# Kernel optimization log

Hardware: AMD Instinct MI355X
Metric: run time of the kernel (lower is better)

The kernel has to match this reference:

```python
import math
import jax, jax.numpy as jnp
from jax import lax
import numpy as np

B, DIM, H, W = 8, 256, 64, 64
D_STATE, D_CONV, EXPAND = 16, 4, 2
D_INNER = EXPAND * DIM
DT_RANK = math.ceil(DIM / 16)
POS_LEN = 16
EPS = 1e-5
GN_GROUPS = 32


def setup_inputs() -> dict:
    key = jax.random.key(0)
    ks = iter(jax.random.split(key, 24))
    rn = lambda shape, s=0.02: jax.random.normal(next(ks), shape, jnp.float32) * s
    inp = {}
    inp["x"] = jax.random.normal(next(ks), (B, DIM, H, W), jnp.float32)
    inp["pos_emb"] = rn((1, DIM, POS_LEN), 1.0)
    inp["ln_g"] = jnp.ones((DIM,), jnp.float32)
    inp["ln_b"] = jnp.zeros((DIM,), jnp.float32)
    inp["m_in_w"] = rn((2, 2 * D_INNER, DIM))
    inp["m_conv_w"] = rn((2, D_INNER, D_CONV), 0.1)
    inp["m_conv_b"] = jnp.zeros((2, D_INNER), jnp.float32)
    inp["m_xproj_w"] = rn((2, DT_RANK + 2 * D_STATE, D_INNER))
    inp["m_dt_w"] = rn((2, D_INNER, DT_RANK), 0.1)
    inp["m_dt_b"] = rn((2, D_INNER), 0.1)
    inp["m_A_log"] = jnp.tile(jnp.log(jnp.arange(1, D_STATE + 1, dtype=jnp.float32))[None, None, :], (2, D_INNER, 1))
    inp["m_D"] = jnp.ones((2, D_INNER), jnp.float32)
    inp["m_out_w"] = rn((2, DIM, D_INNER))
    inp["proj_w"] = rn((DIM, 2 * DIM))
    inp["proj_b"] = jnp.zeros((DIM,), jnp.float32)
    inp["up_dw_w"] = rn((DIM, 1, 3, 3), 0.1)
    inp["up_bn1_g"] = jnp.ones((DIM,), jnp.float32)
    inp["up_bn1_b"] = jnp.zeros((DIM,), jnp.float32)
    inp["up_pw_w"] = rn((DIM, DIM), 0.05)
    inp["up_bn2_g"] = jnp.ones((DIM,), jnp.float32)
    inp["up_bn2_b"] = jnp.zeros((DIM,), jnp.float32)
    inp["down_pw_w"] = rn((DIM, DIM), 0.05)
    inp["down_bn_g"] = jnp.ones((DIM,), jnp.float32)
    inp["down_bn_b"] = jnp.zeros((DIM,), jnp.float32)
    inp["gn_g"] = jnp.ones((DIM,), jnp.float32)
    inp["gn_b"] = jnp.zeros((DIM,), jnp.float32)
    return inp


def reference(x, pos_emb, ln_g, ln_b, m_in_w, m_conv_w, m_conv_b, m_xproj_w, m_dt_w, m_dt_b,
              m_A_log, m_D, m_out_w, proj_w, proj_b, up_dw_w, up_bn1_g, up_bn1_b, up_pw_w,
              up_bn2_g, up_bn2_b, down_pw_w, down_bn_g, down_bn_b, gn_g, gn_b):
    Bx, C, Hh, Ww = x.shape

    def ln(t):  # LayerNorm over last dim (shared self.norm)
        m = jnp.mean(t, -1, keepdims=True)
        v = jnp.mean((t - m) ** 2, -1, keepdims=True)
        return (t - m) * lax.rsqrt(v + EPS) * ln_g + ln_b

    def bn(t, g, b):  # BatchNorm2d in eval mode with default running stats (mean 0, var 1)
        return t * (g / jnp.sqrt(1.0 + EPS))[None, :, None, None] + b[None, :, None, None]

    def gn(t):  # GroupNorm(32, C), shared params (self.bn)
        Bn, Cn, Hn, Wn = t.shape
        tg = t.reshape(Bn, GN_GROUPS, Cn // GN_GROUPS, Hn, Wn)
        m = jnp.mean(tg, (2, 3, 4), keepdims=True)
        v = jnp.mean((tg - m) ** 2, (2, 3, 4), keepdims=True)
        tg = (tg - m) * lax.rsqrt(v + EPS)
        return tg.reshape(Bn, Cn, Hn, Wn) * gn_g[None, :, None, None] + gn_b[None, :, None, None]

    def interp_pos(N):  # F.interpolate(pos_embed, size=N, mode='linear', align_corners=False)
        coords = jnp.maximum((jnp.arange(N, dtype=jnp.float32) + 0.5) * (POS_LEN / N) - 0.5, 0.0)
        i0 = jnp.floor(coords).astype(jnp.int32)
        i1 = jnp.minimum(i0 + 1, POS_LEN - 1)
        wgt = coords - i0.astype(jnp.float32)
        return pos_emb[:, :, i0] * (1.0 - wgt) + pos_emb[:, :, i1] * wgt  # (1,C,N)

    def pe_branch(vals, idx, N):  # vals (B,C,N); indices interp at same size = identity
        t = vals + interp_pos(N) + idx.astype(jnp.float32)
        return ln(jnp.swapaxes(t, 1, 2))  # (B,N,C)

    def mamba(u, d):  # standard mamba_ssm selective scan; u (B,L,C)
        xz = jnp.einsum('blc,ic->bli', u, m_in_w[d])
        xh, zg = jnp.split(xz, 2, -1)
        xc = lax.conv_general_dilated(jnp.swapaxes(xh, 1, 2), m_conv_w[d][:, None, :], (1,),
                                      [(D_CONV - 1, 0)], feature_group_count=D_INNER,
                                      dimension_numbers=('NCH', 'OIH', 'NCH'))
        xc = jnp.swapaxes(jax.nn.silu(xc + m_conv_b[d][None, :, None]), 1, 2)  # (B,L,di)
        dbl = jnp.einsum('bld,ed->ble', xc, m_xproj_w[d])
        dt = dbl[..., :DT_RANK]
        Bm = dbl[..., DT_RANK:DT_RANK + D_STATE]
        Cm = dbl[..., DT_RANK + D_STATE:]
        dt = jax.nn.softplus(jnp.einsum('blr,dr->bld', dt, m_dt_w[d]) + m_dt_b[d])  # (B,L,di)
        A = -jnp.exp(m_A_log[d])  # (di,ds)
        dA = jnp.exp(dt[..., None] * A)  # (B,L,di,ds)
        dBx = dt[..., None] * Bm[:, :, None, :] * xc[..., None]

        def step(h, inps):
            dA_t, dBx_t, C_t = inps
            h = dA_t * h + dBx_t
            return h, jnp.einsum('bds,bs->bd', h, C_t)

        h0 = jnp.zeros((u.shape[0], D_INNER, D_STATE), u.dtype)
        _, ys = lax.scan(step, h0, (jnp.swapaxes(dA, 0, 1), jnp.swapaxes(dBx, 0, 1), jnp.swapaxes(Cm, 0, 1)))
        y = jnp.swapaxes(ys, 0, 1) + xc * m_D[d]
        y = y * jax.nn.silu(zg)
        return jnp.einsum('bld,od->blo', y, m_out_w[d])

    # z branch: depthwise ConvTranspose2d(k3,s2,p1,op1) + BN + ReLU + pw conv + BN, then ReLU6
    z = lax.conv_general_dilated(x, jnp.flip(up_dw_w, (2, 3)), (1, 1), [(1, 2), (1, 2)],
                                 lhs_dilation=(2, 2), feature_group_count=C,
                                 dimension_numbers=('NCHW', 'OIHW', 'NCHW'))  # (B,C,2H,2W)
    z = jax.nn.relu(bn(z, up_bn1_g, up_bn1_b))
    z = jnp.einsum('bchw,oc->bohw', z, up_pw_w)
    z = jnp.clip(bn(z, up_bn2_g, up_bn2_b), 0.0, 6.0)

    col_max = pe_branch(jnp.max(x, 2), jnp.argmax(x, 2), Ww)
    col_min = pe_branch(jnp.min(x, 2), jnp.argmin(x, 2), Ww)
    row_max = pe_branch(jnp.max(x, 3), jnp.argmax(x, 3), Hh)
    row_min = pe_branch(jnp.min(x, 3), jnp.argmin(x, 3), Hh)
    result_max = jnp.concatenate([col_max, row_max], 1)  # (B, W+H, C)
    result_min = jnp.concatenate([col_min, row_min], 1)

    fm_max = ln(mamba(result_max, 0))
    fm_min = ln(mamba(result_min, 0))
    bm_max = ln(mamba(jnp.flip(result_max, 1), 1))
    bm_min = ln(mamba(jnp.flip(result_min, 1), 1))

    res_max = jnp.concatenate([fm_max, jnp.flip(bm_max, 1)], -1) @ proj_w.T + proj_b
    res_min = jnp.concatenate([fm_min, jnp.flip(bm_min, 1)], -1) @ proj_w.T + proj_b
    res_max = ln(res_max)[:, :, None, :]  # (B,L,1,C)
    res_min = ln(res_min)[:, None, :, :]  # (B,1,L,C)

    res = jnp.transpose(res_max + res_min, (0, 3, 1, 2))  # (B,C,L,L), L=H+W=2H
    res = jnp.clip(res + 3.0, 0.0, 6.0) / 6.0 * z  # h_sigmoid gate
    res = gn(res)
    res = jnp.einsum('bchw,oc->bohw', res[:, :, ::2, ::2], down_pw_w)  # pw conv stride 2
    res = bn(res, down_bn_g, down_bn_b)
    res = gn(res)
    res = res + x
    res = gn(res)
    return res
```

## Files before the change

kernel.cpp:

```cpp
#include <hip/hip_runtime.h>
#include <hip/hip_bf16.h>
#include <math.h>

typedef __hip_bfloat16 bf16;
typedef __attribute__((ext_vector_type(8))) short short8_t;
typedef __attribute__((ext_vector_type(4))) short short4_t;
typedef __attribute__((ext_vector_type(4))) float f32x4_t;

#define EPSV 1e-5f
#define BNSC 0.99999500003749968f

__device__ __forceinline__ float bf2f(bf16 v){ return __bfloat162float(v); }
__device__ __forceinline__ bf16 f2bf(float v){ return __float2bfloat16(v); }

__device__ __forceinline__ float blk_sum(float v, float* sm){
  int tid = threadIdx.x;
  #pragma unroll
  for(int o=32;o>0;o>>=1) v += __shfl_down(v, o, 64);
  if((tid&63)==0) sm[tid>>6] = v;
  __syncthreads();
  float s = 0.f;
  int nw = blockDim.x>>6;
  for(int i=0;i<nw;i++) s += sm[i];
  __syncthreads();
  return s;
}

__device__ __forceinline__ float softplusf(float x){
  return (x > 20.f) ? x : __logf(1.f + __expf(x));
}
__device__ __forceinline__ float siluf(float x){
  return x / (1.f + __expf(-x));
}

__global__ void prep_weights(const float* __restrict__ in_w, const float* __restrict__ out_w,
                             const float* __restrict__ pw_w, const float* __restrict__ dpw_w,
                             const float* __restrict__ proj_w,
                             bf16* __restrict__ Winb, bf16* __restrict__ Woutb,
                             bf16* __restrict__ Wub, bf16* __restrict__ Wdb,
                             float* __restrict__ PT, float* __restrict__ gacc){
  int idx = blockIdx.x*256 + threadIdx.x;
  if(idx < 1536) gacc[idx] = 0.f;
  if(idx < 524288){ Winb[idx] = f2bf(in_w[idx]); return; }
  if(idx < 786432){ int i=idx-524288; Woutb[i] = f2bf(out_w[i]); return; }
  if(idx < 851968){ int i=idx-786432; Wub[i] = f2bf(pw_w[i]); return; }
  if(idx < 917504){ int i=idx-851968; Wdb[i] = f2bf(dpw_w[i]); return; }
  int k = idx - 917504;
  int i = k >> 9, j = k & 511;
  PT[j*256 + i] = proj_w[k];
}

__global__ __launch_bounds__(256)
void r1_reduce_pe(const float* __restrict__ x, const float* __restrict__ pe,
                  float* __restrict__ pmax, float* __restrict__ pmin){
  __shared__ float tile[64*65];
  int bc = blockIdx.x;
  int b = bc >> 8, c = bc & 255;
  const float* xp = x + ((size_t)bc << 12);
  for(int i=threadIdx.x; i<4096; i+=256)
    tile[(i>>6)*65 + (i&63)] = xp[i];
  __syncthreads();
  int wv = threadIdx.x >> 6, t = threadIdx.x & 63;
  if(wv >= 2) return;
  float coords = fmaxf((t + 0.5f)*0.25f - 0.5f, 0.f);
  int i0 = (int)floorf(coords);
  int i1 = min(i0+1, 15);
  float wg = coords - (float)i0;
  float pos = pe[c*16+i0]*(1.f-wg) + pe[c*16+i1]*wg;
  if(wv == 0){
    float cmx=-3.4e38f, cmn=3.4e38f; int cax=0, can=0;
    for(int h=0;h<64;h++){
      float v = tile[h*65 + t];
      if(v > cmx){ cmx=v; cax=h; }
      if(v < cmn){ cmn=v; can=h; }
    }
    size_t base_col = ((size_t)b*128 + t)*256 + c;
    pmax[base_col] = cmx + pos + (float)cax;
    pmin[base_col] = cmn + pos + (float)can;
  } else {
    float rmx=-3.4e38f, rmn=3.4e38f; int rax=0, ran=0;
    for(int w=0;w<64;w++){
      float v = tile[t*65 + w];
      if(v > rmx){ rmx=v; rax=w; }
      if(v < rmn){ rmn=v; ran=w; }
    }
    size_t base_row = ((size_t)b*128 + 64 + t)*256 + c;
    pmax[base_row] = rmx + pos + (float)rax;
    pmin[base_row] = rmn + pos + (float)ran;
  }
}

__global__ void ln_rows2(float* __restrict__ bufA, float* __restrict__ bufB,
                         const float* __restrict__ g, const float* __restrict__ bb,
                         bf16* __restrict__ boutA, bf16* __restrict__ boutB){
  __shared__ float sm[8];
  int row = blockIdx.x, t = threadIdx.x;
  float* buf; bf16* bout;
  if(row < 1024){ buf = bufA; bout = boutA; }
  else { buf = bufB; bout = boutB; row -= 1024; }
  float v = buf[(size_t)row*256 + t];
  float m = blk_sum(v, sm) * (1.f/256.f);
  float dv = v - m;
  float var = blk_sum(dv*dv, sm) * (1.f/256.f);
  float r = dv * rsqrtf(var + EPSV) * g[t] + bb[t];
  buf[(size_t)row*256 + t] = r;
  if(bout) bout[(size_t)row*256 + t] = f2bf(r);
}

__global__ __launch_bounds__(256,2)
void m1_mfma(const bf16* __restrict__ ubmax, const bf16* __restrict__ ubmin,
             const bf16* __restrict__ Win, float* __restrict__ xz){
  __shared__ bf16 att[64*264];
  int bx = blockIdx.x;
  int it = bx & 3, lt = (bx>>2)&1, b = (bx>>3)&7, r = bx>>6;
  int d = r & 1;
  const bf16* u = (r < 2) ? ubmax : ubmin;
  int flip = r & 1;
  int t = threadIdx.x;
  {
    int pr = t>>5, cc = (t&31)*8;
    #pragma unroll
    for(int i=0;i<8;i++){
      int p = pr + i*8;
      int l = lt*64 + p;
      int le = flip ? (127 - l) : l;
      short8_t v = *(const short8_t*)((const short*)u + ((size_t)(b*128 + le))*256 + cc);
      *(short8_t*)&att[p*264 + cc] = v;
    }
  }
  __syncthreads();
  int wv = t>>6, lane = t&63, quad = lane>>4, l16 = lane&15;
  int m0 = wv*64;
  f32x4_t acc[4][4];
  #pragma unroll
  for(int ms=0;ms<4;ms++)
    #pragma unroll
    for(int ns=0;ns<4;ns++) acc[ms][ns] = (f32x4_t){0.f,0.f,0.f,0.f};
  const short* wbase = (const short*)Win + ((size_t)d*1024 + it*256)*256;
  for(int k0=0;k0<256;k0+=32){
    short8_t afr[4], bfr[4];
    #pragma unroll
    for(int ms=0;ms<4;ms++)
      afr[ms] = *(const short8_t*)(wbase + (size_t)(m0 + ms*16 + l16)*256 + k0 + quad*8);
    #pragma unroll
    for(int ns=0;ns<4;ns++)
      bfr[ns] = *(const short8_t*)&att[(ns*16 + l16)*264 + k0 + quad*8];
    #pragma unroll
    for(int ms=0;ms<4;ms++)
      #pragma unroll
      for(int ns=0;ns<4;ns++)
        acc[ms][ns] = __builtin_amdgcn_mfma_f32_16x16x32_bf16(afr[ms], bfr[ns], acc[ms][ns], 0,0,0);
  }
  int rb = r*8 + b;
  #pragma unroll
  for(int ns=0;ns<4;ns++){
    int l = lt*64 + ns*16 + l16;
    float* dst = xz + ((size_t)rb*128 + l)*1024 + it*256;
    #pragma unroll
    for(int ms=0;ms<4;ms++){
      int i = m0 + ms*16 + quad*4;
      *(f32x4_t*)(dst + i) = acc[ms][ns];
    }
  }
}

__global__ __launch_bounds__(256)
void m234(const float* __restrict__ xz, const float* __restrict__ cw,
          const float* __restrict__ cb, const float* __restrict__ xproj,
          const float* __restrict__ dtw, const float* __restrict__ dtbias,
          float* __restrict__ xc, float* __restrict__ dbl, float* __restrict__ dt){
  __shared__ float xzs[4*512];
  __shared__ float xcs[512];
  __shared__ float pbuf[192];
  __shared__ float dblrow[48];
  int rowid = blockIdx.x;
  int rb = rowid >> 7, l = rowid & 127;
  int d = (rb >> 3) & 1;
  int t = threadIdx.x;
  #pragma unroll
  for(int i=0;i<8;i++){
    int idx = t + i*256;
    int r = idx >> 9, dd = idx & 511;
    int ls = l - 3 + r;
    xzs[idx] = (ls >= 0) ? xz[((size_t)rb*128 + ls)*1024 + dd] : 0.f;
  }
  __syncthreads();
  #pragma unroll
  for(int i=0;i<2;i++){
    int dd = t + i*256;
    const float* w = cw + (size_t)(d*512 + dd)*4;
    float s = cb[d*512 + dd];
    #pragma unroll
    for(int k=0;k<4;k++) s += xzs[k*512 + dd] * w[k];
    s = siluf(s);
    xcs[dd] = s;
    xc[(size_t)rowid*512 + dd] = s;
  }
  __syncthreads();
  if(t < 192){
    int e = t >> 2, part = t & 3;
    const float* wp = xproj + (size_t)(d*48 + e)*512 + part*128;
    const float* xr = xcs + part*128;
    float s = 0.f;
    for(int k=0;k<128;k++) s += xr[k]*wp[k];
    pbuf[t] = s;
  }
  __syncthreads();
  if(t < 48){
    float s = pbuf[t*4] + pbuf[t*4+1] + pbuf[t*4+2] + pbuf[t*4+3];
    dblrow[t] = s;
    dbl[(size_t)rowid*48 + t] = s;
  }
  __syncthreads();
  #pragma unroll
  for(int i=0;i<2;i++){
    int dd = t + i*256;
    const float* wp = dtw + (size_t)(d*512 + dd)*16;
    float s = dtbias[d*512 + dd];
    #pragma unroll
    for(int r=0;r<16;r++) s += dblrow[r]*wp[r];
    dt[(size_t)rowid*512 + dd] = softplusf(s);
  }
}

__global__ void m5_passA(const float* __restrict__ dt, const float* __restrict__ xc,
                         const float* __restrict__ dbl, const float* __restrict__ Alog,
                         float* __restrict__ P, float* __restrict__ Hl){
  int bx = blockIdx.x;
  int seg = bx & 7, half = (bx>>3)&1, rb = bx>>4;
  int dd = half*256 + threadIdx.x;
  int d = (rb>>3)&1;
  float A[16], h[16], pr[16];
  #pragma unroll
  for(int s=0;s<16;s++){
    A[s] = -__expf(Alog[(size_t)(d*512 + dd)*16 + s]);
    h[s] = 0.f; pr[s] = 1.f;
  }
  int l0 = seg*16;
  for(int l=l0;l<l0+16;l++){
    size_t row = (size_t)rb*128 + l;
    float dtv = dt[row*512 + dd];
    float xcv = xc[row*512 + dd];
    float bx_ = dtv*xcv;
    const float* dr = dbl + row*48;
    #pragma unroll
    for(int s=0;s<16;s++){
      float dA = __expf(dtv*A[s]);
      pr[s] *= dA;
      h[s] = dA*h[s] + bx_*dr[16+s];
    }
  }
  size_t o = ((size_t)(rb*8 + seg)*512 + dd)*16;
  #pragma unroll
  for(int s=0;s<16;s+=4){
    *(f32x4_t*)(P  + o + s) = (f32x4_t){pr[s],pr[s+1],pr[s+2],pr[s+3]};
    *(f32x4_t*)(Hl + o + s) = (f32x4_t){h[s],h[s+1],h[s+2],h[s+3]};
  }
}

__global__ void m5_passB(const float* __restrict__ dt, const float* __restrict__ xc,
                         const float* __restrict__ dbl, const float* __restrict__ xz,
                         const float* __restrict__ Alog, const float* __restrict__ Dp,
                         const float* __restrict__ P, const float* __restrict__ Hl,
                         bf16* __restrict__ ybb){
  int bx = blockIdx.x;
  int seg = bx & 7, half = (bx>>3)&1, rb = bx>>4;
  int dd = half*256 + threadIdx.x;
  int d = (rb>>3)&1;
  float A[16], h[16];
  #pragma unroll
  for(int s=0;s<16;s++){
    A[s] = -__expf(Alog[(size_t)(d*512 + dd)*16 + s]);
    h[s] = 0.f;
  }
  for(int j=0;j<seg;j++){
    size_t o = ((size_t)(rb*8 + j)*512 + dd)*16;
    #pragma unroll
    for(int s=0;s<16;s+=4){
      f32x4_t pv = *(const f32x4_t*)(P + o + s);
      f32x4_t hv = *(const f32x4_t*)(Hl + o + s);
      h[s]   = pv[0]*h[s]   + hv[0];
      h[s+1] = pv[1]*h[s+1] + hv[1];
      h[s+2] = pv[2]*h[s+2] + hv[2];
      h[s+3] = pv[3]*h[s+3] + hv[3];
    }
  }
  float Dv = Dp[d*512 + dd];
  int l0 = seg*16;
  for(int l=l0;l<l0+16;l++){
    size_t row = (size_t)rb*128 + l;
    float dtv = dt[row*512 + dd];
    float xcv = xc[row*512 + dd];
    float zgv = xz[row*1024 + 512 + dd];
    const float* dr = dbl + row*48;
    float bx_ = dtv*xcv;
    float y = 0.f;
    #pragma unroll
    for(int s=0;s<16;s++){
      h[s] = __expf(dtv*A[s])*h[s] + bx_*dr[16+s];
      y += h[s]*dr[32+s];
    }
    ybb[row*512 + dd] = f2bf((y + xcv*Dv) * siluf(zgv));
  }
}

__global__ __launch_bounds__(256,2)
void m6_mfma(const bf16* __restrict__ ybb, const bf16* __restrict__ Wout,
             const float* __restrict__ lng, const float* __restrict__ lnb,
             float* __restrict__ mo){
  __shared__ char smem[64*264*4];
  bf16* ybt = (bf16*)smem;
  float* fbuf = (float*)smem;
  int bx = blockIdx.x;
  int lt = bx & 1, b = (bx>>1)&7, r = bx>>4;
  int d = r & 1, rb = r*8 + b;
  size_t rowbase = (size_t)rb*128 + lt*64;
  int t = threadIdx.x;
  for(int i=t;i<4096;i+=256){
    int row = i>>6, c8 = (i&63)*8;
    short8_t v = *(const short8_t*)((const short*)ybb + (rowbase + row)*512 + c8);
    *(short8_t*)&ybt[row*520 + c8] = v;
  }
  __syncthreads();
  int wv = t>>6, lane = t&63, quad = lane>>4, l16 = lane&15;
  int m0 = wv*64;
  f32x4_t acc[4][4];
  #pragma unroll
  for(int ms=0;ms<4;ms++)
    #pragma unroll
    for(int ns=0;ns<4;ns++) acc[ms][ns] = (f32x4_t){0.f,0.f,0.f,0.f};
  const short* wbase = (const short*)Wout + (size_t)d*256*512;
  for(int k0=0;k0<512;k0+=32){
    short8_t afr[4], bfr[4];
    #pragma unroll
    for(int ms=0;ms<4;ms++)
      afr[ms] = *(const short8_t*)(wbase + (size_t)(m0 + ms*16 + l16)*512 + k0 + quad*8);
    #pragma unroll
    for(int ns=0;ns<4;ns++)
      bfr[ns] = *(const short8_t*)&ybt[(ns*16 + l16)*520 + k0 + quad*8];
    #pragma unroll
    for(int ms=0;ms<4;ms++)
      #pragma unroll
      for(int ns=0;ns<4;ns++)
        acc[ms][ns] = __builtin_amdgcn_mfma_f32_16x16x32_bf16(afr[ms], bfr[ns], acc[ms][ns], 0,0,0);
  }
  __syncthreads();
  #pragma unroll
  for(int ns=0;ns<4;ns++){
    int row = ns*16 + l16;
    #pragma unroll
    for(int ms=0;ms<4;ms++){
      int o = m0 + ms*16 + quad*4;
      *(f32x4_t*)(fbuf + row*264 + o) = acc[ms][ns];
    }
  }
  __syncthreads();
  {
    int row = t >> 2, part = t & 3;
    const float* fr = fbuf + row*264;
    float s = 0.f;
    #pragma unroll 8
    for(int j=0;j<64;j++){
      int col = part*64 + ((j + part*16) & 63);
      s += fr[col];
    }
    s += __shfl_xor(s, 1, 64);
    s += __shfl_xor(s, 2, 64);
    float m = s * (1.f/256.f);
    float q = 0.f;
    #pragma unroll 8
    for(int j=0;j<64;j++){
      int col = part*64 + ((j + part*16) & 63);
      float dv = fr[col] - m;
      q += dv*dv;
    }
    q += __shfl_xor(q, 1, 64);
    q += __shfl_xor(q, 2, 64);
    float rs = rsqrtf(q*(1.f/256.f) + EPSV);
    float* dst = mo + (rowbase + row)*256;
    for(int j=0;j<64;j++){
      int col = part*64 + j;
      dst[col] = (fr[col] - m)*rs*lng[col] + lnb[col];
    }
  }
}

__global__ void m7_proj(const float* __restrict__ mo, const float* __restrict__ PT,
                        const float* __restrict__ pb, const float* __restrict__ lng,
                        const float* __restrict__ lnb, float* __restrict__ resm,
                        float* __restrict__ resn){
  __shared__ float ct[16*512];
  __shared__ float fbuf[16*264];
  int bx = blockIdx.x;
  int tt = bx >> 6, rem = bx & 63, b = rem >> 3, lt = rem & 7;
  int fr_ = tt*2, br = tt*2 + 1;
  for(int i=threadIdx.x;i<16*512;i+=256){
    int lr = i >> 9, k = i & 511;
    int l = lt*16 + lr;
    ct[i] = (k < 256)
      ? mo[(((size_t)(fr_*8+b)*128) + l)*256 + k]
      : mo[(((size_t)(br*8+b)*128) + (127-l))*256 + (k-256)];
  }
  __syncthreads();
  float acc[16];
  #pragma unroll
  for(int q=0;q<16;q++) acc[q] = 0.f;
  int t = threadIdx.x;
  for(int k=0;k<512;k++){
    float pv = PT[(size_t)k*256 + t];
    #pragma unroll
    for(int q=0;q<16;q++) acc[q] += pv * ct[(q<<9) + k];
  }
  float bias = pb[t];
  #pragma unroll
  for(int q=0;q<16;q++) fbuf[q*264 + t] = acc[q] + bias;
  __syncthreads();
  float* dstbuf = tt ? resn : resm;
  if(t < 64){
    int row = t >> 2, part = t & 3;
    const float* fr = fbuf + row*264;
    float s = 0.f;
    for(int j=0;j<64;j++){
      int col = part*64 + ((j + part*16) & 63);
      s += fr[col];
    }
    s += __shfl_xor(s, 1, 64);
    s += __shfl_xor(s, 2, 64);
    float m = s * (1.f/256.f);
    float q = 0.f;
    for(int j=0;j<64;j++){
      int col = part*64 + ((j + part*16) & 63);
      float dv = fr[col] - m;
      q += dv*dv;
    }
    q += __shfl_xor(q, 1, 64);
    q += __shfl_xor(q, 2, 64);
    float rs = rsqrtf(q*(1.f/256.f) + EPSV);
    float* dst = dstbuf + ((size_t)b*128 + lt*16 + row)*256;
    for(int j=0;j<64;j++){
      int col = part*64 + j;
      dst[col] = (fr[col] - m)*rs*lng[col] + lnb[col];
    }
  }
}

__global__ __launch_bounds__(256)
void k1_deconv_T(const float* __restrict__ x, const float* __restrict__ wdw,
                 const float* __restrict__ g1, const float* __restrict__ b1,
                 bf16* __restrict__ zT){
  __shared__ float in[2*64*33];
  __shared__ bf16 ot[64*80];
  int bx = blockIdx.x;
  int cb = bx & 3, half = (bx>>2)&1, h = (bx>>3)&127, b = bx>>10;
  int c0 = cb*64, w0 = half*64, iw0 = w0>>1;
  int h_odd = h & 1;
  int ihA = h_odd ? (h-1)>>1 : h>>1;
  int ihB = (h+1)>>1;
  bool hasB = h_odd && (ihB < 64);
  for(int i = threadIdx.x; i < 4224; i += 256){
    int row = i / 2112;
    int rem = i - row*2112;
    int c = rem / 33;
    int iw = rem - c*33;
    int ihl = row ? ihB : ihA;
    bool valid = (iw0 + iw < 64) && (row == 0 || hasB);
    in[i] = valid ? x[(((size_t)b*256 + c0 + c)<<12) + (ihl<<6) + iw0 + iw] : 0.f;
  }
  __syncthreads();
  int c = threadIdx.x & 63, g = threadIdx.x >> 6;
  const float* wp = wdw + (c0+c)*9;
  int khA3 = h_odd ? 6 : 3;
  float wA0 = wp[khA3], wA1 = wp[khA3+1], wA2 = wp[khA3+2];
  float wB0 = wp[0],    wB1 = wp[1],      wB2 = wp[2];
  float scale = g1[c0+c]*BNSC, bias = b1[c0+c];
  const float* inA = in + c*33;
  const float* inB = in + 2112 + c*33;
  #pragma unroll
  for(int i=0;i<16;i++){
    int wi = g*16 + i;
    float s;
    if(!(i&1)){
      int iw = wi>>1;
      s = inA[iw]*wA1 + inB[iw]*wB1;
    } else {
      int iwa = (wi-1)>>1, iwb = (wi+1)>>1;
      s = inA[iwa]*wA2 + inA[iwb]*wA0 + inB[iwa]*wB2 + inB[iwb]*wB0;
    }
    ot[wi*80 + c] = f2bf(fmaxf(s*scale + bias, 0.f));
  }
  __syncthreads();
  int rr = threadIdx.x >> 3;
  int co = (threadIdx.x & 7) * 8;
  size_t obase = (((size_t)b*16384) + (size_t)h*128 + w0)*256 + c0;
  #pragma unroll
  for(int pass=0; pass<2; pass++){
    int wi = rr + pass*32;
    short8_t v = *(const short8_t*)&ot[wi*80 + co];
    *(short8_t*)((short*)zT + obase + (size_t)wi*256 + co) = v;
  }
}

__global__ __launch_bounds__(256,2)
void k2_mfma(const bf16* __restrict__ zT, const bf16* __restrict__ Wub,
             const float* __restrict__ g2, const float* __restrict__ b2,
             const float* __restrict__ resm, const float* __restrict__ resn,
             bf16* __restrict__ resT){
  __shared__ bf16 zt[128*264];
  int b = blockIdx.y;
  int p0 = blockIdx.x*128;
  int t = threadIdx.x;
  {
    const short* src = (const short*)zT + (((size_t)b*16384 + p0)*256);
    int pr = t>>5;
    int cc = (t&31)*8;
    #pragma unroll
    for(int i=0;i<16;i++){
      int p = pr + i*8;
      short8_t v = *(const short8_t*)(src + (size_t)p*256 + cc);
      *(short8_t*)&zt[p*264 + cc] = v;
    }
  }
  __syncthreads();
  int wv = t>>6, lane = t&63, quad = lane>>4, l16 = lane&15;
  int m0 = wv*64;
  f32x4_t acc[4][8];
  #pragma unroll
  for(int ms=0;ms<4;ms++)
    #pragma unroll
    for(int ns=0;ns<8;ns++) acc[ms][ns] = (f32x4_t){0.f,0.f,0.f,0.f};
  const short* wp = (const short*)Wub + (size_t)(m0 + l16)*256 + quad*8;
  short8_t afr[4];
  #pragma unroll
  for(int ms=0;ms<4;ms++) afr[ms] = *(const short8_t*)(wp + (size_t)ms*16*256);
  for(int k0=0;k0<256;k0+=32){
    short8_t anext[4];
    if(k0 + 32 < 256){
      #pragma unroll
      for(int ms=0;ms<4;ms++)
        anext[ms] = *(const short8_t*)(wp + (size_t)ms*16*256 + k0 + 32);
    }
    short8_t bfr[8];
    #pragma unroll
    for(int ns=0;ns<8;ns++)
      bfr[ns] = *(const short8_t*)&zt[(ns*16 + l16)*264 + k0 + quad*8];
    #pragma unroll
    for(int ms=0;ms<4;ms++)
      #pragma unroll
      for(int ns=0;ns<8;ns++)
        acc[ms][ns] = __builtin_amdgcn_mfma_f32_16x16x32_bf16(afr[ms], bfr[ns], acc[ms][ns], 0,0,0);
    #pragma unroll
    for(int ms=0;ms<4;ms++) afr[ms] = anext[ms];
  }
  __syncthreads();
  #pragma unroll
  for(int ns=0;ns<8;ns++){
    int pl = ns*16 + l16;
    int p = p0 + pl;
    int hh = p>>7, ww = p&127;
    const float* rm = resm + ((size_t)b*128+hh)*256;
    const float* rn = resn + ((size_t)b*128+ww)*256;
    #pragma unroll
    for(int ms=0;ms<4;ms++){
      int o = m0 + ms*16 + quad*4;
      f32x4_t a = acc[ms][ns];
      f32x4_t gv = *(const f32x4_t*)(g2+o);
      f32x4_t bv = *(const f32x4_t*)(b2+o);
      f32x4_t rmv = *(const f32x4_t*)(rm+o);
      f32x4_t rnv = *(const f32x4_t*)(rn+o);
      alignas(8) bf16 ov[4];
      #pragma unroll
      for(int r=0;r<4;r++){
        float zv = a[r]*(gv[r]*BNSC) + bv[r];
        zv = fminf(fmaxf(zv, 0.f), 6.f);
        float gate = fminf(fmaxf(rmv[r]+rnv[r]+3.f, 0.f), 6.f)*(1.f/6.f);
        ov[r] = f2bf(zv*gate);
      }
      *(short4_t*)&zt[pl*264 + o] = *(const short4_t*)ov;
    }
  }
  __syncthreads();
  {
    short* dst = (short*)resT + ((size_t)b*16384 + p0)*256;
    int slot0 = t;
    #pragma unroll
    for(int it=0; it<16; it++){
      int slot = slot0 + it*256;
      int row = slot >> 5;
      int co = (slot & 31)*8;
      short8_t v = *(const short8_t*)&zt[row*264 + co];
      *(short8_t*)(dst + (size_t)row*256 + co) = v;
    }
  }
}

__global__ void gn_stats_pm(const bf16* __restrict__ resT, float* __restrict__ sum,
                            float* __restrict__ ssq){
  __shared__ float ls[256], lq[256];
  int b = blockIdx.y, p0 = blockIdx.x*256;
  int c = threadIdx.x;
  const short* src = (const short*)resT + ((size_t)b*16384 + p0)*256 + c;
  float s=0.f, q=0.f;
  for(int i=0;i<256;i++){
    bf16 raw; *(short*)&raw = src[(size_t)i*256];
    float v = bf2f(raw);
    s += v; q += v*v;
  }
  ls[c]=s; lq[c]=q;
  __syncthreads();
  if(c<32){
    float S=0.f,Q=0.f;
    #pragma unroll
    for(int j=0;j<8;j++){ S+=ls[c*8+j]; Q+=lq[c*8+j]; }
    atomicAdd(&sum[b*32+c], S);
    atomicAdd(&ssq[b*32+c], Q);
  }
}

__global__ __launch_bounds__(256,2)
void k4_mfma(const bf16* __restrict__ resT, const bf16* __restrict__ Wdb,
             const float* __restrict__ gsum1, const float* __restrict__ gssq1,
             const float* __restrict__ gng, const float* __restrict__ gnb,
             const float* __restrict__ dbg, const float* __restrict__ dbb,
             float* __restrict__ t1, float* __restrict__ gsum2, float* __restrict__ gssq2){
  __shared__ bf16 at[128*264];
  __shared__ float sc[256], sb[256];
  __shared__ float stm[32], str[32];
  int b = blockIdx.y;
  int q0 = blockIdx.x*128;
  int t = threadIdx.x;
  if(t < 32){
    float m = gsum1[b*32+t] * (1.f/131072.f);
    float var = gssq1[b*32+t] * (1.f/131072.f) - m*m;
    stm[t] = m;
    str[t] = rsqrtf(var + EPSV);
  }
  __syncthreads();
  {
    int cch = t, g = cch>>3;
    float m = stm[g], rs = str[g];
    float s = rs*gng[cch];
    sc[cch] = s; sb[cch] = gnb[cch] - m*s;
  }
  __syncthreads();
  {
    int pr = t>>5;
    int cc = (t&31)*8;
    #pragma unroll
    for(int i=0;i<16;i++){
      int q = pr + i*8;
      int qq = q0 + q;
      int y = qq>>6, xw = qq&63;
      size_t srow = ((size_t)b*16384 + (size_t)y*256 + xw*2)*256;
      short8_t v = *(const short8_t*)((const short*)resT + srow + cc);
      const bf16* vv = (const bf16*)&v;
      alignas(16) bf16 ov[8];
      #pragma unroll
      for(int j=0;j<8;j++) ov[j] = f2bf(bf2f(vv[j])*sc[cc+j] + sb[cc+j]);
      *(short8_t*)&at[q*264 + cc] = *(const short8_t*)ov;
    }
  }
  __syncthreads();
  int wv = t>>6, lane = t&63, quad = lane>>4, l16 = lane&15;
  int n0 = wv*64;
  f32x4_t acc[8][4];
  #pragma unroll
  for(int ms=0;ms<8;ms++)
    #pragma unroll
    for(int ns=0;ns<4;ns++) acc[ms][ns] = (f32x4_t){0.f,0.f,0.f,0.f};
  const short* wp = (const short*)Wdb + (size_t)(n0 + l16)*256 + quad*8;
  short8_t bfr[4];
  #pragma unroll
  for(int ns=0;ns<4;ns++) bfr[ns] = *(const short8_t*)(wp + (size_t)ns*16*256);
  for(int k0=0;k0<256;k0+=32){
    short8_t bnext[4];
    if(k0 + 32 < 256){
      #pragma unroll
      for(int ns=0;ns<4;ns++)
        bnext[ns] = *(const short8_t*)(wp + (size_t)ns*16*256 + k0 + 32);
    }
    short8_t afr[8];
    #pragma unroll
    for(int ms=0;ms<8;ms++)
      afr[ms] = *(const short8_t*)&at[(ms*16 + l16)*264 + k0 + quad*8];
    #pragma unroll
    for(int ms=0;ms<8;ms++)
      #pragma unroll
      for(int ns=0;ns<4;ns++)
        acc[ms][ns] = __builtin_amdgcn_mfma_f32_16x16x32_bf16(afr[ms], bfr[ns], acc[ms][ns], 0,0,0);
    #pragma unroll
    for(int ns=0;ns<4;ns++) bfr[ns] = bnext[ns];
  }
  #pragma unroll
  for(int ns=0;ns<4;ns++){
    int o = n0 + ns*16 + l16;
    float s2 = dbg[o]*BNSC, bb2 = dbb[o];
    float* dst = t1 + (((size_t)b*256 + o) << 12);
    float s_=0.f, q_=0.f;
    #pragma unroll
    for(int ms=0;ms<8;ms++){
      int ps = q0 + ms*16 + quad*4;
      f32x4_t a = acc[ms][ns];
      f32x4_t ov;
      #pragma unroll
      for(int r=0;r<4;r++){
        ov[r] = a[r]*s2 + bb2;
        s_ += ov[r];
        q_ += ov[r]*ov[r];
      }
      *(f32x4_t*)(dst + ps) = ov;
    }
    #pragma unroll
    for(int msk=1; msk<=4; msk<<=1){
      s_ += __shfl_xor(s_, msk, 64);
      q_ += __shfl_xor(q_, msk, 64);
    }
    s_ += __shfl_xor(s_, 16, 64);
    q_ += __shfl_xor(q_, 16, 64);
    s_ += __shfl_xor(s_, 32, 64);
    q_ += __shfl_xor(q_, 32, 64);
    if(((l16 & 7) == 0) && (quad == 0)){
      atomicAdd(&gsum2[b*32 + (o>>3)], s_);
      atomicAdd(&gssq2[b*32 + (o>>3)], q_);
    }
  }
}

__global__ void k6_gn_add(float* __restrict__ t1, const float* __restrict__ x,
                          const float* __restrict__ gsum2, const float* __restrict__ gssq2,
                          const float* __restrict__ gng, const float* __restrict__ gnb,
                          float* __restrict__ gsum3, float* __restrict__ gssq3){
  __shared__ float sm[8];
  int i4 = blockIdx.x*256 + threadIdx.x;
  int idx = i4 << 2;
  int c = (idx >> 12) & 255, b = idx >> 20, g = c >> 3;
  float m2 = gsum2[b*32+g] * (1.f/32768.f);
  float var = gssq2[b*32+g] * (1.f/32768.f) - m2*m2;
  float rs = rsqrtf(var + EPSV);
  float scl = rs*gng[c], off = gnb[c] - m2*scl;
  f32x4_t tv = *(const f32x4_t*)(t1 + idx);
  f32x4_t xv = *(const f32x4_t*)(x + idx);
  f32x4_t ov;
  float S = 0.f, Q = 0.f;
  #pragma unroll
  for(int r=0;r<4;r++){
    float v = tv[r]*scl + off + xv[r];
    ov[r] = v;
    S += v; Q += v*v;
  }
  *(f32x4_t*)(t1 + idx) = ov;
  S = blk_sum(S, sm);
  Q = blk_sum(Q, sm);
  if(threadIdx.x == 0){
    atomicAdd(&gsum3[b*32 + g], S);
    atomicAdd(&gssq3[b*32 + g], Q);
  }
}

__global__ void k8_gn_out(const float* __restrict__ t1, const float* __restrict__ gsum3,
                          const float* __restrict__ gssq3, const float* __restrict__ gng,
                          const float* __restrict__ gnb, float* __restrict__ out){
  int i4 = blockIdx.x*256 + threadIdx.x;
  int idx = i4 << 2;
  int c = (idx >> 12) & 255, b = idx >> 20, g = c >> 3;
  float m = gsum3[b*32+g] * (1.f/32768.f);
  float var = gssq3[b*32+g] * (1.f/32768.f) - m*m;
  float rs = rsqrtf(var + EPSV);
  float scl = rs*gng[c], off = gnb[c] - m*scl;
  f32x4_t tv = *(const f32x4_t*)(t1 + idx);
  f32x4_t ov;
  #pragma unroll
  for(int r=0;r<4;r++) ov[r] = tv[r]*scl + off;
  *(f32x4_t*)(out + idx) = ov;
}

extern "C" void kernel_launch(void* const* d_in, const int* in_sizes, int n_in,
                              void* d_out, int out_size, void* d_ws, size_t ws_size,
                              hipStream_t stream){
  const float* x      = (const float*)d_in[0];
  const float* pos    = (const float*)d_in[1];
  const float* ln_g   = (const float*)d_in[2];
  const float* ln_b   = (const float*)d_in[3];
  const float* in_w   = (const float*)d_in[4];
  const float* conv_w = (const float*)d_in[5];
  const float* conv_b = (const float*)d_in[6];
  const float* xproj  = (const float*)d_in[7];
  const float* dt_w   = (const float*)d_in[8];
  const float* dt_b   = (const float*)d_in[9];
  const float* A_log  = (const float*)d_in[10];
  const float* Dp     = (const float*)d_in[11];
  const float* out_w  = (const float*)d_in[12];
  const float* proj_w = (const float*)d_in[13];
  const float* proj_b = (const float*)d_in[14];
  const float* dw_w   = (const float*)d_in[15];
  const float* bn1g   = (const float*)d_in[16];
  const float* bn1b   = (const float*)d_in[17];
  const float* pw_w   = (const float*)d_in[18];
  const float* bn2g   = (const float*)d_in[19];
  const float* bn2b   = (const float*)d_in[20];
  const float* dpw_w  = (const float*)d_in[21];
  const float* dbng   = (const float*)d_in[22];
  const float* dbnb   = (const float*)d_in[23];
  const float* gng    = (const float*)d_in[24];
  const float* gnb    = (const float*)d_in[25];
  float* out = (float*)d_out;

  float* ws = (float*)d_ws;
  bf16*  resT = (bf16*)ws;
  bf16*  zT   = (bf16*)(ws + 16777216);
  float* scanP = ws + 16777216;
  float* scanH = ws + 16777216 + 2097152;
  float* zone = ws + 33554432;
  float* xz   = zone;
  float* xc   = xz  + 4194304;
  float* dbl  = xc  + 2097152;
  float* dtb  = dbl + 196608;
  bf16*  ybb  = (bf16*)(dtb + 2097152);
  float* t1   = zone;
  float* mo   = zone + 9633792;
  float* resm = mo   + 1048576;
  float* resn = resm + 262144;
  float* pmax = resn + 262144;
  float* pmin = pmax + 262144;
  float* PT   = pmin + 262144;
  bf16*  ubmax= (bf16*)(PT + 131072);
  bf16*  ubmin= (bf16*)(PT + 131072 + 131072);
  bf16*  Winb = (bf16*)(PT + 131072 + 262144);
  bf16*  Woutb= (bf16*)(PT + 131072 + 524288);
  bf16*  Wub  = (bf16*)(PT + 131072 + 655360);
  bf16*  Wdb  = (bf16*)(PT + 131072 + 688128);
  float* gacc = PT + 131072 + 720896;
  float* gsum1 = gacc,        *gssq1 = gacc + 256;
  float* gsum2 = gacc + 512,  *gssq2 = gacc + 768;
  float* gsum3 = gacc + 1024, *gssq3 = gacc + 1280;

  prep_weights<<<4096,256,0,stream>>>(in_w, out_w, pw_w, dpw_w, proj_w,
                                      Winb, Woutb, Wub, Wdb, PT, gacc);

  r1_reduce_pe<<<2048,256,0,stream>>>(x, pos, pmax, pmin);
  ln_rows2<<<2048,256,0,stream>>>(pmax, pmin, ln_g, ln_b, ubmax, ubmin);

  m1_mfma<<<256,256,0,stream>>>(ubmax, ubmin, Winb, xz);
  m234<<<4096,256,0,stream>>>(xz, conv_w, conv_b, xproj, dt_w, dt_b, xc, dbl, dtb);
  m5_passA<<<512,256,0,stream>>>(dtb, xc, dbl, A_log, scanP, scanH);
  m5_passB<<<512,256,0,stream>>>(dtb, xc, dbl, xz, A_log, Dp, scanP, scanH, ybb);
  m6_mfma<<<64,256,0,stream>>>(ybb, Woutb, ln_g, ln_b, mo);
  m7_proj<<<128,256,0,stream>>>(mo, PT, proj_b, ln_g, ln_b, resm, resn);

  k1_deconv_T<<<8192,256,0,stream>>>(x, dw_w, bn1g, bn1b, zT);
  k2_mfma<<<dim3(128,8),256,0,stream>>>(zT, Wub, bn2g, bn2b, resm, resn, resT);
  gn_stats_pm<<<dim3(64,8),256,0,stream>>>(resT, gsum1, gssq1);

  k4_mfma<<<dim3(32,8),256,0,stream>>>(resT, Wdb, gsum1, gssq1,
                                       gng, gnb, dbng, dbnb, t1, gsum2, gssq2);

  k6_gn_add<<<8192,256,0,stream>>>(t1, x, gsum2, gssq2, gng, gnb, gsum3, gssq3);
  k8_gn_out<<<8192,256,0,stream>>>(t1, gsum3, gssq3, gng, gnb, out);
}
```

Measured before the change: 522.9 us.

## Process eight sequence positions per block in fused conv/xproj/dt kernel

The m234 kernel now handles a segment of 8 consecutive rows per block instead of one row. The overlapping conv window loads are shared, and the xproj and dt weights are reused across rows. The inner dot products use float4 vector loads. Grid size drops from 4096 to 512 blocks, which gives less parallelism and uses more shared memory per block (about 42KB) in exchange for fewer redundant loads.

```diff
diff --git a/kernel.cpp b/kernel.cpp
--- a/kernel.cpp
+++ b/kernel.cpp
@@ -164,62 +164,82 @@
   }
 }
 
+#define LSEG 8
 __global__ __launch_bounds__(256)
 void m234(const float* __restrict__ xz, const float* __restrict__ cw,
           const float* __restrict__ cb, const float* __restrict__ xproj,
           const float* __restrict__ dtw, const float* __restrict__ dtbias,
           float* __restrict__ xc, float* __restrict__ dbl, float* __restrict__ dt){
-  __shared__ float xzs[4*512];
-  __shared__ float xcs[512];
-  __shared__ float pbuf[192];
-  __shared__ float dblrow[48];
-  int rowid = blockIdx.x;
-  int rb = rowid >> 7, l = rowid & 127;
+  __shared__ float xzs[(LSEG+3)*512];
+  __shared__ float xcs[LSEG*512];
+  __shared__ float pbuf[LSEG*96];
+  __shared__ float dblrow[LSEG*48];
+  int bx = blockIdx.x;
+  int rb = bx >> 4, seg = bx & 15;
+  int l0 = seg * LSEG;
   int d = (rb >> 3) & 1;
   int t = threadIdx.x;
   #pragma unroll
-  for(int i=0;i<8;i++){
-    int idx = t + i*256;
-    int r = idx >> 9, dd = idx & 511;
-    int ls = l - 3 + r;
-    xzs[idx] = (ls >= 0) ? xz[((size_t)rb*128 + ls)*1024 + dd] : 0.f;
-  }
-  __syncthreads();
-  #pragma unroll
-  for(int i=0;i<2;i++){
-    int dd = t + i*256;
-    const float* w = cw + (size_t)(d*512 + dd)*4;
+  for(int j=0; j<(LSEG+3)*512/256; j++){
+    int i = t + j*256;
+    int r = i >> 9, dd = i & 511;
+    int ls = l0 - 3 + r;
+    xzs[i] = (ls >= 0) ? xz[((size_t)rb*128 + ls)*1024 + dd] : 0.f;
+  }
+  __syncthreads();
+  #pragma unroll
+  for(int j=0; j<(LSEG*512)/256; j++){
+    int i = t + j*256;
+    int lr = i >> 9, dd = i & 511;
+    f32x4_t wv = *(const f32x4_t*)(cw + (size_t)(d*512 + dd)*4);
     float s = cb[d*512 + dd];
-    #pragma unroll
-    for(int k=0;k<4;k++) s += xzs[k*512 + dd] * w[k];
+    s += xzs[(lr+0)*512 + dd]*wv[0];
+    s += xzs[(lr+1)*512 + dd]*wv[1];
+    s += xzs[(lr+2)*512 + dd]*wv[2];
+    s += xzs[(lr+3)*512 + dd]*wv[3];
     s = siluf(s);
-    xcs[dd] = s;
-    xc[(size_t)rowid*512 + dd] = s;
-  }
-  __syncthreads();
-  if(t < 192){
-    int e = t >> 2, part = t & 3;
-    const float* wp = xproj + (size_t)(d*48 + e)*512 + part*128;
-    const float* xr = xcs + part*128;
+    xcs[i] = s;
+    xc[((size_t)(rb*128 + l0 + lr))*512 + dd] = s;
+  }
+  __syncthreads();
+  #pragma unroll
+  for(int j=0; j<3; j++){
+    int id = t + j*256;
+    int row = id / 96;
+    int rem = id - row*96;
+    int e = rem >> 1, part = rem & 1;
+    const float* wp = xproj + ((size_t)(d*48 + e)*512) + part*256;
+    const float* xr = xcs + row*512 + part*256;
     float s = 0.f;
-    for(int k=0;k<128;k++) s += xr[k]*wp[k];
-    pbuf[t] = s;
-  }
-  __syncthreads();
-  if(t < 48){
-    float s = pbuf[t*4] + pbuf[t*4+1] + pbuf[t*4+2] + pbuf[t*4+3];
-    dblrow[t] = s;
-    dbl[(size_t)rowid*48 + t] = s;
-  }
-  __syncthreads();
-  #pragma unroll
-  for(int i=0;i<2;i++){
-    int dd = t + i*256;
+    #pragma unroll 4
+    for(int k4=0; k4<64; k4++){
+      f32x4_t wv = *(const f32x4_t*)(wp + k4*4);
+      f32x4_t xv = *(const f32x4_t*)(xr + k4*4);
+      s += wv[0]*xv[0] + wv[1]*xv[1] + wv[2]*xv[2] + wv[3]*xv[3];
+    }
+    pbuf[id] = s;
+  }
+  __syncthreads();
+  for(int i=t; i<LSEG*48; i+=256){
+    float s = pbuf[2*i] + pbuf[2*i+1];
+    dblrow[i] = s;
+    int row = i / 48, e = i - row*48;
+    dbl[((size_t)(rb*128 + l0 + row))*48 + e] = s;
+  }
+  __syncthreads();
+  #pragma unroll
+  for(int j=0; j<(LSEG*512)/256; j++){
+    int i = t + j*256;
+    int row = i >> 9, dd = i & 511;
     const float* wp = dtw + (size_t)(d*512 + dd)*16;
+    const float* dr = dblrow + row*48;
     float s = dtbias[d*512 + dd];
     #pragma unroll
-    for(int r=0;r<16;r++) s += dblrow[r]*wp[r];
-    dt[(size_t)rowid*512 + dd] = softplusf(s);
+    for(int r4=0; r4<4; r4++){
+      f32x4_t wv = *(const f32x4_t*)(wp + r4*4);
+      s += dr[r4*4+0]*wv[0] + dr[r4*4+1]*wv[1] + dr[r4*4+2]*wv[2] + dr[r4*4+3]*wv[3];
+    }
+    dt[((size_t)(rb*128 + l0 + row))*512 + dd] = softplusf(s);
   }
 }
 
@@ -840,7 +860,7 @@
   ln_rows2<<<2048,256,0,stream>>>(pmax, pmin, ln_g, ln_b, ubmax, ubmin);
 
   m1_mfma<<<256,256,0,stream>>>(ubmax, ubmin, Winb, xz);
-  m234<<<4096,256,0,stream>>>(xz, conv_w, conv_b, xproj, dt_w, dt_b, xc, dbl, dtb);
+  m234<<<512,256,0,stream>>>(xz, conv_w, conv_b, xproj, dt_w, dt_b, xc, dbl, dtb);
   m5_passA<<<512,256,0,stream>>>(dtb, xc, dbl, A_log, scanP, scanH);
   m5_passB<<<512,256,0,stream>>>(dtb, xc, dbl, xz, A_log, Dp, scanP, scanH, ybb);
   m6_mfma<<<64,256,0,stream>>>(ybb, Woutb, ln_g, ln_b, mo);
```

After: 510.4 us. 1.02x faster.
